# Optimization experiments

Measured on AMD Instinct MI355X. Metric: run time of the kernel, lower is better.

The kernel has to match this reference:

```python
import jax, jax.numpy as jnp
import numpy as np

B, N, C, H = 4, 4096, 1024, 16
D = C // H


def setup_inputs() -> dict:
    key = jax.random.key(0)
    ks = jax.random.split(key, 15)
    s = 0.02
    f = lambda k, shp: jax.random.normal(k, shp, dtype=jnp.float32) * s
    return {
        "x": f(ks[0], (B, N, C)),
        "qkv_w": f(ks[1], (C, 3 * C)),
        "qkv_b": f(ks[2], (3 * C,)),
        "out_w": f(ks[3], (C, C)),
        "out_b": f(ks[4], (C,)),
        # NB: original code dynamically re-creates position_bias as (1, N, H, H)
        # because q/k/v are never transposed to (B,H,N,D); attention runs over heads.
        "pos_bias": f(ks[5], (1, N, H, H)),
        "conv_w": f(ks[6], (C, C)),
        "conv_b": f(ks[7], (C,)),
        "pw_w": f(ks[8], (C, C, 1)),   # Conv1d kernel_size=1: (out, in, k)
        "pw_b": f(ks[9], (C,)),
        "dw_w": f(ks[10], (C, 1, 3)),  # depthwise Conv1d groups=C: (out, in/groups=1, k)
        "dw_b": f(ks[11], (C,)),
        "tok_w": f(ks[12], (C, C)),
        "tok_b": f(ks[13], (C,)),
    }


def reference(x, qkv_w, qkv_b, out_w, out_b, pos_bias,
              conv_w, conv_b, pw_w, pw_b, dw_w, dw_b, tok_w, tok_b):
    b, n, c = x.shape
    h = pos_bias.shape[2]
    d = c // h
    scale = d ** (-0.5)

    # ---- attention branch (faithful to source: heads axis is attended over) ----
    qkv = (x @ qkv_w + qkv_b).reshape(b, n, h, 3 * d)
    q, k, v = jnp.split(qkv, 3, axis=-1)  # each (B, N, H, D)
    scores = jnp.einsum("bnhd,bngd->bnhg", q, k) * scale + pos_bias  # (B, N, H, H)
    attn_w = jax.nn.softmax(scores, axis=-1)
    attn = jnp.einsum("bnhg,bngd->bnhd", attn_w, v).reshape(b, n, c)
    attn = attn @ out_w + out_b

    # ---- convolutional branch ----
    xc = x @ conv_w + conv_b            # (B, N, C)
    xc = xc.transpose(0, 2, 1)          # (B, C, N)
    dn = ("NCH", "OIH", "NCH")
    xc = jax.lax.conv_general_dilated(xc, pw_w, (1,), [(0, 0)],
                                      dimension_numbers=dn) + pw_b[None, :, None]
    xc = jax.lax.conv_general_dilated(xc, dw_w, (1,), [(1, 1)],
                                      dimension_numbers=dn,
                                      feature_group_count=c) + dw_b[None, :, None]
    xc = xc.transpose(0, 2, 1) @ tok_w + tok_b  # (B, N, C)

    return attn + xc
```

## Files before the change

### kernel.cpp

```cpp
#include <hip/hip_runtime.h>
#include <hip/hip_bf16.h>


typedef __attribute__((ext_vector_type(8))) short sh8;
typedef __attribute__((ext_vector_type(4))) float f4;

__device__ __forceinline__ float bf2f(short s) {
  unsigned u = ((unsigned)(unsigned short)s) << 16;
  return __builtin_bit_cast(float, u);
}
__device__ __forceinline__ short f2bf(float f) {
  return __builtin_bit_cast(short, __float2bfloat16(f));
}
__device__ __forceinline__ void g2l16(const void* g, void* l) {
  __builtin_amdgcn_global_load_lds(
      (const __attribute__((address_space(1))) unsigned int*)g,
      (__attribute__((address_space(3))) unsigned int*)l, 16, 0, 0);
}

__global__ __launch_bounds__(256) void cvt3(
    const float* __restrict__ x, const float* __restrict__ conv_w,
    const float* __restrict__ pw_w, short* __restrict__ xb,
    short* __restrict__ convb, short* __restrict__ pwb) {
  int i = blockIdx.x * 256 + threadIdx.x;
  const float* src;
  short* dst;
  int off;
  if (i < 2097152) {
    src = x; dst = xb; off = i;
  } else if (i < 2228224) {
    src = conv_w; dst = convb; off = i - 2097152;
  } else {
    src = pw_w; dst = pwb; off = i - 2228224;
  }
  float4 a = ((const float4*)src)[off * 2];
  float4 b = ((const float4*)src)[off * 2 + 1];
  sh8 o;
  o[0] = f2bf(a.x); o[1] = f2bf(a.y); o[2] = f2bf(a.z); o[3] = f2bf(a.w);
  o[4] = f2bf(b.x); o[5] = f2bf(b.y); o[6] = f2bf(b.z); o[7] = f2bf(b.w);
  ((sh8*)dst)[off] = o;
}

__global__ __launch_bounds__(256) void transpose_f32_bf16(
    const float* __restrict__ src, short* __restrict__ dst,
    int N, int ldd, int coff) {
  __shared__ float tile[32][33];
  int kb = blockIdx.y * 32, nb = blockIdx.x * 32;
  int tx = threadIdx.x, ty = threadIdx.y;
#pragma unroll
  for (int j = 0; j < 32; j += 8)
    tile[ty + j][tx] = src[(size_t)(kb + ty + j) * N + nb + tx];
  __syncthreads();
#pragma unroll
  for (int j = 0; j < 32; j += 8)
    dst[(size_t)(nb + ty + j) * ldd + coff + kb + tx] = f2bf(tile[tx][ty + j]);
}

__global__ __launch_bounds__(256) void transpose2(
    const float* __restrict__ out_w, const float* __restrict__ tok_w,
    short* __restrict__ dst) {
  __shared__ float tile[32][33];
  const float* src = blockIdx.z ? tok_w : out_w;
  int coff = blockIdx.z ? 1024 : 0;
  int kb = blockIdx.y * 32, nb = blockIdx.x * 32;
  int tx = threadIdx.x, ty = threadIdx.y;
#pragma unroll
  for (int j = 0; j < 32; j += 8)
    tile[ty + j][tx] = src[(size_t)(kb + ty + j) * 1024 + nb + tx];
  __syncthreads();
#pragma unroll
  for (int j = 0; j < 32; j += 8)
    dst[(size_t)(nb + ty + j) * 2048 + coff + kb + tx] = f2bf(tile[tx][ty + j]);
}

__global__ __launch_bounds__(256) void prep_misc(
    const float* __restrict__ pw_w, const float* __restrict__ conv_b,
    const float* __restrict__ pw_b, const float* __restrict__ qkv_b,
    const float* __restrict__ out_b, const float* __restrict__ tok_b,
    const float* __restrict__ dw_w, const float* __restrict__ dw_b,
    float* __restrict__ bias4, float* __restrict__ bcat,
    float* __restrict__ dw0, float* __restrict__ dw1,
    float* __restrict__ dw2, float* __restrict__ dwb) {
  int o = blockIdx.x;
  if (o < 1024) {
    float part = 0.f;
    for (int i = threadIdx.x; i < 1024; i += 256)
      part += pw_w[(size_t)o * 1024 + i] * conv_b[i];
#pragma unroll
    for (int off = 32; off >= 1; off >>= 1) part += __shfl_down(part, off);
    __shared__ float red[4];
    int wid = threadIdx.x >> 6, lane = threadIdx.x & 63;
    if (lane == 0) red[wid] = part;
    __syncthreads();
    if (threadIdx.x == 0) {
      float s = red[0] + red[1] + red[2] + red[3];
      bias4[3072 + o] = s + pw_b[o];
      bcat[o] = out_b[o] + tok_b[o];
      dw0[o] = dw_w[o * 3 + 0];
      dw1[o] = dw_w[o * 3 + 1];
      dw2[o] = dw_w[o * 3 + 2];
      dwb[o] = dw_b[o];
    }
  }
  if (threadIdx.x == 0) bias4[o] = qkv_b[o];
}

template <int OUT_BF16>
__global__ __launch_bounds__(256, 2) void gemm128(
    const short* __restrict__ A, const short* __restrict__ Bt,
    void* __restrict__ Cp, const float* __restrict__ bias, int K, int ldc) {
  __shared__ short As[128 * 32];
  __shared__ short Bs[128 * 32];
  const int wid = threadIdx.x >> 6, lane = threadIdx.x & 63;
  const int bm = blockIdx.y, bn = blockIdx.x;
  const int wr = wid >> 1, wc = wid & 1;
  const size_t abase = (size_t)bm * 128 * K;
  const size_t bbase = (size_t)bn * 128 * K;
  const int r16 = lane & 15, ko = (lane >> 4) * 8;

  f4 acc[4][4] = {};

  for (int k0 = 0; k0 < K; k0 += 32) {
    __syncthreads();
#pragma unroll
    for (int c = 0; c < 2; ++c) {
      int ch = c * 256 + wid * 64 + lane;
      int row = ch >> 2, kc = (ch & 3) * 8;
      g2l16(A + abase + (size_t)row * K + k0 + kc, &As[ch * 8]);
      g2l16(Bt + bbase + (size_t)row * K + k0 + kc, &Bs[ch * 8]);
    }
    __syncthreads();
    sh8 af[4], bf[4];
#pragma unroll
    for (int i = 0; i < 4; ++i)
      af[i] = *(const sh8*)&As[(wr * 64 + i * 16 + r16) * 32 + ko];
#pragma unroll
    for (int j = 0; j < 4; ++j)
      bf[j] = *(const sh8*)&Bs[(wc * 64 + j * 16 + r16) * 32 + ko];
#pragma unroll
    for (int i = 0; i < 4; ++i)
#pragma unroll
      for (int j = 0; j < 4; ++j)
        acc[i][j] = __builtin_amdgcn_mfma_f32_16x16x32_bf16(af[i], bf[j],
                                                            acc[i][j], 0, 0, 0);
  }

  const int crow = wr * 64 + (lane >> 4) * 4;
  const int ccol = wc * 64 + r16;
#pragma unroll
  for (int i = 0; i < 4; ++i) {
#pragma unroll
    for (int j = 0; j < 4; ++j) {
      int col = bn * 128 + ccol + j * 16;
      float bv = bias ? bias[col] : 0.f;
#pragma unroll
      for (int r = 0; r < 4; ++r) {
        int row = bm * 128 + crow + i * 16 + r;
        float v = acc[i][j][r] + bv;
        if (OUT_BF16)
          ((short*)Cp)[(size_t)row * ldc + col] = f2bf(v);
        else
          ((float*)Cp)[(size_t)row * ldc + col] = v;
      }
    }
  }
}

template <int OUT_BF16>
__global__ __launch_bounds__(512, 2) void gemm256(
    const short* __restrict__ A, const short* __restrict__ Bt,
    void* __restrict__ Cp, const float* __restrict__ bias,
    int K, int ldc, int nbn) {
  __shared__ short lds[65536];
  const int tid = threadIdx.x;
  const int lane = tid & 63, wid = tid >> 6;
  const int wr = wid >> 2, wc = wid & 3;
  const int r16 = lane & 15;
  const int kidx = ((lane >> 4) ^ ((r16 >> 1) & 3)) << 3;

  const int cpx = gridDim.x >> 3;
  const int swz = (blockIdx.x & 7) * cpx + (blockIdx.x >> 3);
  const int bm = swz / nbn, bn = swz % nbn;

  const short* Ag = A + (size_t)bm * 256 * K;
  const short* Bg = Bt + (size_t)bn * 256 * K;

  int goff0, goff1, loff0, loff1;
  {
    int s0 = tid, row0 = s0 >> 2;
    int kc0 = (s0 & 3) ^ ((row0 >> 1) & 3);
    goff0 = row0 * K + kc0 * 8;
    loff0 = s0 * 8;
    int s1 = 512 + tid, row1 = s1 >> 2;
    int kc1 = (s1 & 3) ^ ((row1 >> 1) & 3);
    goff1 = row1 * K + kc1 * 8;
    loff1 = s1 * 8;
  }

  f4 acc[8][4] = {};
  const int NT = K >> 5;

#define STAGE_FULL(KT, B)                                   \
  do {                                                      \
    short* lb = &lds[(B) * 16384];                          \
    const short* ga = Ag + (KT) * 32;                       \
    const short* gb = Bg + (KT) * 32;                       \
    g2l16(ga + goff0, lb + loff0);                          \
    g2l16(gb + goff0, lb + 8192 + loff0);                   \
    g2l16(ga + goff1, lb + loff1);                          \
    g2l16(gb + goff1, lb + 8192 + loff1);                   \
  } while (0)

#define LOADFRAG(AF, BF, BUFIDX)                                          \
  do {                                                                    \
    const short* Ab_ = &lds[(BUFIDX) * 16384];                            \
    const short* Bb_ = Ab_ + 8192;                                        \
    _Pragma("unroll")                                                     \
    for (int i = 0; i < 8; ++i)                                           \
      AF[i] = *(const sh8*)&Ab_[(wr * 128 + i * 16 + r16) * 32 + kidx];   \
    _Pragma("unroll")                                                     \
    for (int j = 0; j < 4; ++j)                                           \
      BF[j] = *(const sh8*)&Bb_[(wc * 64 + j * 16 + r16) * 32 + kidx];    \
  } while (0)

#define MFMA_ALL(AF, BF)                                                  \
  do {                                                                    \
    _Pragma("unroll")                                                     \
    for (int i = 0; i < 8; ++i)                                           \
      _Pragma("unroll")                                                   \
      for (int j = 0; j < 4; ++j)                                         \
        acc[i][j] = __builtin_amdgcn_mfma_f32_16x16x32_bf16(              \
            AF[i], BF[j], acc[i][j], 0, 0, 0);                            \
  } while (0)

  STAGE_FULL(0, 0);
  STAGE_FULL(1, 1);
  STAGE_FULL(2, 2);
  asm volatile("s_waitcnt vmcnt(4)" ::: "memory");
  __builtin_amdgcn_sched_barrier(0);
  __builtin_amdgcn_s_barrier();
  __builtin_amdgcn_sched_barrier(0);

  sh8 afA[8], bfA[4], afB[8], bfB[4];
  LOADFRAG(afA, bfA, 0);

  for (int t = 0; t < NT; t += 2) {
    LOADFRAG(afB, bfB, (t + 1) & 3);
    {
      const int kt = (t + 3 < NT) ? t + 3 : 0;
      STAGE_FULL(kt, (t + 3) & 3);
    }
    __builtin_amdgcn_s_setprio(1);
    MFMA_ALL(afA, bfA);
    __builtin_amdgcn_s_setprio(0);
    __builtin_amdgcn_sched_barrier(0);
    asm volatile("s_waitcnt vmcnt(4)" ::: "memory");
    __builtin_amdgcn_sched_barrier(0);
    __builtin_amdgcn_s_barrier();
    __builtin_amdgcn_sched_barrier(0);

    LOADFRAG(afA, bfA, (t + 2) & 3);
    {
      const int kt = (t + 4 < NT) ? t + 4 : 0;
      STAGE_FULL(kt, (t + 4) & 3);
    }
    __builtin_amdgcn_s_setprio(1);
    MFMA_ALL(afB, bfB);
    __builtin_amdgcn_s_setprio(0);
    __builtin_amdgcn_sched_barrier(0);
    asm volatile("s_waitcnt vmcnt(4)" ::: "memory");
    __builtin_amdgcn_sched_barrier(0);
    __builtin_amdgcn_s_barrier();
    __builtin_amdgcn_sched_barrier(0);
  }
#undef STAGE_FULL
#undef LOADFRAG
#undef MFMA_ALL

  const int crow0 = bm * 256 + wr * 128 + (lane >> 4) * 4;
  const int ccol0 = bn * 256 + wc * 64 + r16;
  float bv[4];
#pragma unroll
  for (int j = 0; j < 4; ++j) bv[j] = bias ? bias[ccol0 + j * 16] : 0.f;
#pragma unroll
  for (int i = 0; i < 8; ++i) {
#pragma unroll
    for (int r = 0; r < 4; ++r) {
      size_t rowoff = (size_t)(crow0 + i * 16 + r) * ldc + ccol0;
#pragma unroll
      for (int j = 0; j < 4; ++j) {
        float v = acc[i][j][r] + bv[j];
        if (OUT_BF16)
          ((short*)Cp)[rowoff + j * 16] = f2bf(v);
        else
          ((float*)Cp)[rowoff + j * 16] = v;
      }
    }
  }
}

__global__ __launch_bounds__(256) void epilogue(
    const short* __restrict__ qkvx, const float* __restrict__ pos_bias,
    const float* __restrict__ dw0, const float* __restrict__ dw1,
    const float* __restrict__ dw2, const float* __restrict__ dwb,
    short* __restrict__ xcat) {
  __shared__ short sq[4 * 3072];
  __shared__ short slice[6 * 1024];
  int t0 = blockIdx.x * 4;
#pragma unroll
  for (int c = 0; c < 6; ++c) {
    int g = c * 256 + threadIdx.x;
    int tok = (g * 683) >> 18;
    int off = g - tok * 384;
    ((sh8*)sq)[tok * 384 + off] =
        *(const sh8*)(qkvx + (size_t)(t0 + tok) * 4096 + off * 8);
  }
#pragma unroll
  for (int s = 0; s < 3; ++s) {
    int g = s * 256 + threadIdx.x;
    int r = g >> 7, off = g & 127;
    int gr = t0 - 1 + r;
    sh8 v = {};
    if (gr >= 0 && gr < 16384)
      v = *(const sh8*)(qkvx + (size_t)gr * 4096 + 3072 + off * 8);
    ((sh8*)slice)[g] = v;
  }
  __syncthreads();

  int wid = threadIdx.x >> 6, lane = threadIdx.x & 63;
  int t = t0 + wid, n = t & 4095;
  int h = lane >> 2, sub = lane & 3;
  const short* base = sq + wid * 3072 + h * 192;

  float qf[64];
#pragma unroll
  for (int c = 0; c < 8; ++c) {
    sh8 v8 = *(const sh8*)(base + c * 8);
#pragma unroll
    for (int j = 0; j < 8; ++j) qf[c * 8 + j] = bf2f(v8[j]);
  }

  const float* pb = pos_bias + (size_t)n * 256 + h * 16 + sub * 4;
  float p[4];
  float m = -1e30f;
#pragma unroll
  for (int g4 = 0; g4 < 4; ++g4) {
    int g = sub * 4 + g4;
    const short* kk = sq + wid * 3072 + g * 192 + 64;
    float acc = 0.f;
#pragma unroll
    for (int c = 0; c < 8; ++c) {
      sh8 k8 = *(const sh8*)(kk + c * 8);
#pragma unroll
      for (int j = 0; j < 8; ++j) acc += qf[c * 8 + j] * bf2f(k8[j]);
    }
    p[g4] = acc * 0.125f + pb[g4];
    m = fmaxf(m, p[g4]);
  }
  m = fmaxf(m, __shfl_xor(m, 1));
  m = fmaxf(m, __shfl_xor(m, 2));
  float sum = 0.f;
#pragma unroll
  for (int g4 = 0; g4 < 4; ++g4) {
    p[g4] = __expf(p[g4] - m);
    sum += p[g4];
  }
  sum += __shfl_xor(sum, 1);
  sum += __shfl_xor(sum, 2);
  float inv = 1.0f / sum;
#pragma unroll
  for (int g4 = 0; g4 < 4; ++g4) p[g4] *= inv;

  float pall[16];
#pragma unroll
  for (int g = 0; g < 16; ++g)
    pall[g] = __shfl(p[g & 3], (lane & 60) | (g >> 2));

  float o[16] = {};
#pragma unroll
  for (int g = 0; g < 16; ++g) {
    const short* vv = sq + wid * 3072 + g * 192 + 128 + sub * 16;
    sh8 va = *(const sh8*)vv;
    sh8 vb = *(const sh8*)(vv + 8);
#pragma unroll
    for (int j = 0; j < 8; ++j) {
      o[j] += pall[g] * bf2f(va[j]);
      o[8 + j] += pall[g] * bf2f(vb[j]);
    }
  }
  sh8 oa, ob;
#pragma unroll
  for (int j = 0; j < 8; ++j) {
    oa[j] = f2bf(o[j]);
    ob[j] = f2bf(o[8 + j]);
  }
  short* dst = xcat + (size_t)t * 2048 + h * 64 + sub * 16;
  *(sh8*)dst = oa;
  *(sh8*)(dst + 8) = ob;

#pragma unroll
  for (int it = 0; it < 2; ++it) {
    int w = it * 256 + threadIdx.x;
    int tok = w >> 7, co = (w & 127) * 8;
    int tt = t0 + tok, nn = tt & 4095;
    const short* lo8 = slice + tok * 1024 + co;
    const short* mi8 = lo8 + 1024;
    const short* hi8 = lo8 + 2048;
    sh8 lo = (nn > 0) ? *(const sh8*)lo8 : sh8{};
    sh8 mi = *(const sh8*)mi8;
    sh8 hi = (nn < 4095) ? *(const sh8*)hi8 : sh8{};
    sh8 out;
#pragma unroll
    for (int j = 0; j < 8; ++j) {
      float v = dw0[co + j] * bf2f(lo[j]) + dw1[co + j] * bf2f(mi[j]) +
                dw2[co + j] * bf2f(hi[j]) + dwb[co + j];
      out[j] = f2bf(v);
    }
    *(sh8*)(xcat + (size_t)tt * 2048 + 1024 + co) = out;
  }
}

extern "C" void kernel_launch(void* const* d_in, const int* in_sizes, int n_in,
                              void* d_out, int out_size, void* d_ws,
                              size_t ws_size, hipStream_t stream) {
  const float* x      = (const float*)d_in[0];
  const float* qkv_w  = (const float*)d_in[1];
  const float* qkv_b  = (const float*)d_in[2];
  const float* out_w  = (const float*)d_in[3];
  const float* out_b  = (const float*)d_in[4];
  const float* pos_b  = (const float*)d_in[5];
  const float* conv_w = (const float*)d_in[6];
  const float* conv_b = (const float*)d_in[7];
  const float* pw_w   = (const float*)d_in[8];
  const float* pw_b   = (const float*)d_in[9];
  const float* dw_w   = (const float*)d_in[10];
  const float* dw_b   = (const float*)d_in[11];
  const float* tok_w  = (const float*)d_in[12];
  const float* tok_b  = (const float*)d_in[13];

  const int M = 16384;
  char* ws = (char*)d_ws;
  size_t off = 0;
  auto alloc = [&](size_t bytes) -> void* {
    void* p = ws + off;
    off += (bytes + 255) & ~(size_t)255;
    return p;
  };
  short* xb    = (short*)alloc((size_t)M * 1024 * 2);
  short* wbig  = (short*)alloc((size_t)4096 * 1024 * 2);
  short* wcatT = (short*)alloc((size_t)1024 * 2048 * 2);
  short* convb = (short*)alloc((size_t)1024 * 1024 * 2);
  short* pwb   = (short*)alloc((size_t)1024 * 1024 * 2);
  short* qkvx  = (short*)alloc((size_t)M * 4096 * 2);
  short* xcat  = (short*)alloc((size_t)M * 2048 * 2);
  float* bias4 = (float*)alloc(4096 * 4);
  float* bcat  = (float*)alloc(1024 * 4);
  float* dw0   = (float*)alloc(1024 * 4);
  float* dw1   = (float*)alloc(1024 * 4);
  float* dw2   = (float*)alloc(1024 * 4);
  float* dwb   = (float*)alloc(1024 * 4);
  (void)ws_size; (void)in_sizes; (void)n_in; (void)out_size;

  cvt3<<<9216, 256, 0, stream>>>(x, conv_w, pw_w, xb, convb, pwb);
  transpose_f32_bf16<<<dim3(96, 32), dim3(32, 8), 0, stream>>>(qkv_w, wbig, 3072, 1024, 0);
  transpose2<<<dim3(32, 32, 2), dim3(32, 8), 0, stream>>>(out_w, tok_w, wcatT);
  prep_misc<<<3072, 256, 0, stream>>>(pw_w, conv_b, pw_b, qkv_b, out_b, tok_b,
                                      dw_w, dw_b, bias4, bcat, dw0, dw1, dw2, dwb);
  gemm128<1><<<dim3(8, 8), 256, 0, stream>>>(pwb, convb, wbig + (size_t)3072 * 1024,
                                             nullptr, 1024, 1024);

  gemm256<1><<<1024, 512, 0, stream>>>(xb, wbig, qkvx, bias4, 1024, 4096, 16);

  epilogue<<<4096, 256, 0, stream>>>(qkvx, pos_b, dw0, dw1, dw2, dwb, xcat);

  gemm256<0><<<256, 512, 0, stream>>>(xcat, wcatT, d_out, bcat, 2048, 1024, 4);
}
```

Measured before the change: 318.8 us.

## Compute per-token head attention with MFMA and merge weight transposes

Replaces the scalar FMA loops for the per-token 16x16 head-attention scores and the probability-times-V product with bf16 16x16x32 MFMA instructions. Q/K/V are staged into padded shared memory and V is transposed in LDS so it can feed the MFMA B operand. Softmax reductions move to cross-lane shuffles that match the MFMA output layout. The two weight-transpose kernels are also fused into one launch. Probabilities are now rounded to bf16 before the PV product, which slightly lowers precision, and the extra LDS traffic and padding add cost.

```diff
diff --git a/kernel.cpp b/kernel.cpp
--- a/kernel.cpp
+++ b/kernel.cpp
@@ -3,6 +3,7 @@
 
 
 typedef __attribute__((ext_vector_type(8))) short sh8;
+typedef __attribute__((ext_vector_type(4))) short sh4;
 typedef __attribute__((ext_vector_type(4))) float f4;
 
 __device__ __forceinline__ float bf2f(short s) {
@@ -41,11 +42,26 @@
   ((sh8*)dst)[off] = o;
 }
 
-__global__ __launch_bounds__(256) void transpose_f32_bf16(
-    const float* __restrict__ src, short* __restrict__ dst,
-    int N, int ldd, int coff) {
+__global__ __launch_bounds__(256) void transpose3(
+    const float* __restrict__ qkv_w, const float* __restrict__ out_w,
+    const float* __restrict__ tok_w, short* __restrict__ wbig,
+    short* __restrict__ wcatT) {
   __shared__ float tile[32][33];
-  int kb = blockIdx.y * 32, nb = blockIdx.x * 32;
+  int z = blockIdx.z;
+  const float* src;
+  short* dst;
+  int N, ldd, coff, nb;
+  if (z < 3) {
+    src = qkv_w; dst = wbig; N = 3072; ldd = 1024; coff = 0;
+    nb = z * 1024 + blockIdx.x * 32;
+  } else if (z == 3) {
+    src = out_w; dst = wcatT; N = 1024; ldd = 2048; coff = 0;
+    nb = blockIdx.x * 32;
+  } else {
+    src = tok_w; dst = wcatT; N = 1024; ldd = 2048; coff = 1024;
+    nb = blockIdx.x * 32;
+  }
+  int kb = blockIdx.y * 32;
   int tx = threadIdx.x, ty = threadIdx.y;
 #pragma unroll
   for (int j = 0; j < 32; j += 8)
@@ -54,23 +70,6 @@
 #pragma unroll
   for (int j = 0; j < 32; j += 8)
     dst[(size_t)(nb + ty + j) * ldd + coff + kb + tx] = f2bf(tile[tx][ty + j]);
-}
-
-__global__ __launch_bounds__(256) void transpose2(
-    const float* __restrict__ out_w, const float* __restrict__ tok_w,
-    short* __restrict__ dst) {
-  __shared__ float tile[32][33];
-  const float* src = blockIdx.z ? tok_w : out_w;
-  int coff = blockIdx.z ? 1024 : 0;
-  int kb = blockIdx.y * 32, nb = blockIdx.x * 32;
-  int tx = threadIdx.x, ty = threadIdx.y;
-#pragma unroll
-  for (int j = 0; j < 32; j += 8)
-    tile[ty + j][tx] = src[(size_t)(kb + ty + j) * 1024 + nb + tx];
-  __syncthreads();
-#pragma unroll
-  for (int j = 0; j < 32; j += 8)
-    dst[(size_t)(nb + ty + j) * 2048 + coff + kb + tx] = f2bf(tile[tx][ty + j]);
 }
 
 __global__ __launch_bounds__(256) void prep_misc(
@@ -304,16 +303,18 @@
     const float* __restrict__ dw0, const float* __restrict__ dw1,
     const float* __restrict__ dw2, const float* __restrict__ dwb,
     short* __restrict__ xcat) {
-  __shared__ short sq[4 * 3072];
+  __shared__ short sq[4 * 3328];
   __shared__ short slice[6 * 1024];
+  __shared__ short vT[4 * 1536];
   int t0 = blockIdx.x * 4;
 #pragma unroll
-  for (int c = 0; c < 6; ++c) {
-    int g = c * 256 + threadIdx.x;
+  for (int it = 0; it < 6; ++it) {
+    int g = it * 256 + threadIdx.x;
     int tok = (g * 683) >> 18;
-    int off = g - tok * 384;
-    ((sh8*)sq)[tok * 384 + off] =
-        *(const sh8*)(qkvx + (size_t)(t0 + tok) * 4096 + off * 8);
+    int c = g - tok * 384;
+    int hd = c / 24, wi = c - hd * 24;
+    *(sh8*)(sq + tok * 3328 + hd * 208 + wi * 8) =
+        *(const sh8*)(qkvx + (size_t)(t0 + tok) * 4096 + c * 8);
   }
 #pragma unroll
   for (int s = 0; s < 3; ++s) {
@@ -329,74 +330,72 @@
 
   int wid = threadIdx.x >> 6, lane = threadIdx.x & 63;
   int t = t0 + wid, n = t & 4095;
-  int h = lane >> 2, sub = lane & 3;
-  const short* base = sq + wid * 3072 + h * 192;
-
-  float qf[64];
-#pragma unroll
-  for (int c = 0; c < 8; ++c) {
-    sh8 v8 = *(const sh8*)(base + c * 8);
-#pragma unroll
-    for (int j = 0; j < 8; ++j) qf[c * 8 + j] = bf2f(v8[j]);
-  }
-
-  const float* pb = pos_bias + (size_t)n * 256 + h * 16 + sub * 4;
-  float p[4];
+  int lg = lane & 15, lk = lane >> 4;
+  const short* tb = sq + wid * 3328;
+  short* vt = vT + wid * 1536;
+
+  {
+    int d = lane;
+    short tmp[16];
+#pragma unroll
+    for (int g = 0; g < 16; ++g) tmp[g] = tb[g * 208 + 128 + d];
+#pragma unroll
+    for (int g0 = 0; g0 < 16; g0 += 4)
+      *(sh4*)(vt + d * 24 + g0) = *(const sh4*)&tmp[g0];
+  }
+
+  f4 s = {};
+  {
+    sh8 kf0 = *(const sh8*)(tb + lg * 208 + 64 + lk * 8);
+    sh8 qf0 = *(const sh8*)(tb + lg * 208 + lk * 8);
+    s = __builtin_amdgcn_mfma_f32_16x16x32_bf16(kf0, qf0, s, 0, 0, 0);
+    sh8 kf1 = *(const sh8*)(tb + lg * 208 + 96 + lk * 8);
+    sh8 qf1 = *(const sh8*)(tb + lg * 208 + 32 + lk * 8);
+    s = __builtin_amdgcn_mfma_f32_16x16x32_bf16(kf1, qf1, s, 0, 0, 0);
+  }
+
+  f4 pbv = *(const f4*)(pos_bias + (size_t)n * 256 + lg * 16 + lk * 4);
+  float e[4];
   float m = -1e30f;
 #pragma unroll
-  for (int g4 = 0; g4 < 4; ++g4) {
-    int g = sub * 4 + g4;
-    const short* kk = sq + wid * 3072 + g * 192 + 64;
-    float acc = 0.f;
-#pragma unroll
-    for (int c = 0; c < 8; ++c) {
-      sh8 k8 = *(const sh8*)(kk + c * 8);
-#pragma unroll
-      for (int j = 0; j < 8; ++j) acc += qf[c * 8 + j] * bf2f(k8[j]);
-    }
-    p[g4] = acc * 0.125f + pb[g4];
-    m = fmaxf(m, p[g4]);
-  }
-  m = fmaxf(m, __shfl_xor(m, 1));
-  m = fmaxf(m, __shfl_xor(m, 2));
+  for (int r = 0; r < 4; ++r) {
+    e[r] = s[r] * 0.125f + pbv[r];
+    m = fmaxf(m, e[r]);
+  }
+  m = fmaxf(m, __shfl_xor(m, 16));
+  m = fmaxf(m, __shfl_xor(m, 32));
   float sum = 0.f;
 #pragma unroll
-  for (int g4 = 0; g4 < 4; ++g4) {
-    p[g4] = __expf(p[g4] - m);
-    sum += p[g4];
-  }
-  sum += __shfl_xor(sum, 1);
-  sum += __shfl_xor(sum, 2);
+  for (int r = 0; r < 4; ++r) {
+    e[r] = __expf(e[r] - m);
+    sum += e[r];
+  }
+  sum += __shfl_xor(sum, 16);
+  sum += __shfl_xor(sum, 32);
   float inv = 1.0f / sum;
 #pragma unroll
-  for (int g4 = 0; g4 < 4; ++g4) p[g4] *= inv;
-
-  float pall[16];
-#pragma unroll
-  for (int g = 0; g < 16; ++g)
-    pall[g] = __shfl(p[g & 3], (lane & 60) | (g >> 2));
-
-  float o[16] = {};
-#pragma unroll
-  for (int g = 0; g < 16; ++g) {
-    const short* vv = sq + wid * 3072 + g * 192 + 128 + sub * 16;
-    sh8 va = *(const sh8*)vv;
-    sh8 vb = *(const sh8*)(vv + 8);
-#pragma unroll
-    for (int j = 0; j < 8; ++j) {
-      o[j] += pall[g] * bf2f(va[j]);
-      o[8 + j] += pall[g] * bf2f(vb[j]);
-    }
-  }
-  sh8 oa, ob;
+  for (int r = 0; r < 4; ++r) e[r] *= inv;
+
+  sh8 ap;
 #pragma unroll
   for (int j = 0; j < 8; ++j) {
-    oa[j] = f2bf(o[j]);
-    ob[j] = f2bf(o[8 + j]);
-  }
-  short* dst = xcat + (size_t)t * 2048 + h * 64 + sub * 16;
-  *(sh8*)dst = oa;
-  *(sh8*)(dst + 8) = ob;
+    float pv_ = __shfl(e[j & 3], (((lk & 1) * 2 + (j >> 2)) * 16) + lg);
+    ap[j] = (lk < 2) ? f2bf(pv_) : (short)0;
+  }
+
+  f4 pv[4] = {};
+#pragma unroll
+  for (int c = 0; c < 4; ++c) {
+    sh8 bf = *(const sh8*)(vt + (c * 16 + lg) * 24 + (lk & 1) * 8);
+    pv[c] = __builtin_amdgcn_mfma_f32_16x16x32_bf16(ap, bf, pv[c], 0, 0, 0);
+  }
+
+  short* dst = xcat + (size_t)t * 2048;
+#pragma unroll
+  for (int c = 0; c < 4; ++c)
+#pragma unroll
+    for (int r = 0; r < 4; ++r)
+      dst[(lk * 4 + r) * 64 + c * 16 + lg] = f2bf(pv[c][r]);
 
 #pragma unroll
   for (int it = 0; it < 2; ++it) {
@@ -462,8 +461,8 @@
   (void)ws_size; (void)in_sizes; (void)n_in; (void)out_size;
 
   cvt3<<<9216, 256, 0, stream>>>(x, conv_w, pw_w, xb, convb, pwb);
-  transpose_f32_bf16<<<dim3(96, 32), dim3(32, 8), 0, stream>>>(qkv_w, wbig, 3072, 1024, 0);
-  transpose2<<<dim3(32, 32, 2), dim3(32, 8), 0, stream>>>(out_w, tok_w, wcatT);
+  transpose3<<<dim3(32, 32, 5), dim3(32, 8), 0, stream>>>(qkv_w, out_w, tok_w,
+                                                          wbig, wcatT);
   prep_misc<<<3072, 256, 0, stream>>>(pw_w, conv_b, pw_b, qkv_b, out_b, tok_b,
                                       dw_w, dw_b, bias4, bcat, dw0, dw1, dw2, dwb);
   gemm128<1><<<dim3(8, 8), 256, 0, stream>>>(pwb, convb, wbig + (size_t)3072 * 1024,
```

Result: faster. 307.1 us (-3.7%).
